# Optimization experiments

Hardware: AMD Instinct MI355X
Metric: run time of the kernel (lower is better)

## Reference

```python
import jax, jax.numpy as jnp
import numpy as np

QUERY_DIM = 512
KV_DIM = 64
N_AUX = 8
B = 65536
EPS = 1e-5


def setup_inputs() -> dict:
    key = jax.random.key(0)
    k1, k2, k3, k4, k5 = jax.random.split(key, 5)
    query = jax.random.normal(k1, (B, QUERY_DIM), dtype=jnp.float32)
    kv_stack = jax.random.normal(k2, (B, N_AUX, KV_DIM), dtype=jnp.float32)
    # Linear weights (torch nn.Linear stores W as [out, in]; y = x @ W.T)
    w_q = jax.random.normal(k3, (KV_DIM, QUERY_DIM), dtype=jnp.float32) / np.sqrt(QUERY_DIM)
    w_k = jax.random.normal(k4, (KV_DIM, KV_DIM), dtype=jnp.float32) / np.sqrt(KV_DIM)
    w_v = jax.random.normal(k5, (KV_DIM, KV_DIM), dtype=jnp.float32) / np.sqrt(KV_DIM)
    ln_gamma = jnp.ones((KV_DIM,), dtype=jnp.float32)
    ln_beta = jnp.zeros((KV_DIM,), dtype=jnp.float32)
    return {"query": query, "kv_stack": kv_stack, "w_q": w_q, "w_k": w_k,
            "w_v": w_v, "ln_gamma": ln_gamma, "ln_beta": ln_beta}


def reference(query, kv_stack, w_q, w_k, w_v, ln_gamma, ln_beta):
    scale = KV_DIM ** (-0.5)
    q = query @ w_q.T                                  # (B, kv_dim)
    k = jnp.einsum('bnd,ed->bne', kv_stack, w_k)       # (B, n_aux, kv_dim)
    v = jnp.einsum('bnd,ed->bne', kv_stack, w_v)       # (B, n_aux, kv_dim)
    scores = jnp.einsum('bd,bnd->bn', q, k) * scale    # (B, n_aux)
    attn_w = jax.nn.softmax(scores, axis=-1)
    out = jnp.einsum('bn,bnd->bd', attn_w, v)          # (B, kv_dim)
    # LayerNorm over last dim
    mu = jnp.mean(out, axis=-1, keepdims=True)
    var = jnp.var(out, axis=-1, keepdims=True)
    normed = (out - mu) / jnp.sqrt(var + EPS)
    return normed * ln_gamma + ln_beta
```

## Files before the change

### kernel.cpp

```cpp
#include <hip/hip_runtime.h>

#define QD 512
#define KD 64
#define NROWS 64
#define LDA 136
#define LDT 68
#define LDU 72

typedef __attribute__((ext_vector_type(8))) short short8;
typedef __attribute__((ext_vector_type(4))) float f32x4;
typedef __attribute__((ext_vector_type(4))) unsigned short u16x4;

static __device__ __forceinline__ unsigned short f2bf(float f) {
  unsigned u = __builtin_bit_cast(unsigned, f);
  u += 0x7FFFu + ((u >> 16) & 1u);
  return (unsigned short)(u >> 16);
}
static __device__ __forceinline__ float bf2f(unsigned short s) {
  return __builtin_bit_cast(float, (unsigned)s << 16);
}
static __device__ __forceinline__ short8 pack8(f32x4 a, f32x4 b) {
  short8 r;
  r[0] = (short)f2bf(a[0]); r[1] = (short)f2bf(a[1]);
  r[2] = (short)f2bf(a[2]); r[3] = (short)f2bf(a[3]);
  r[4] = (short)f2bf(b[0]); r[5] = (short)f2bf(b[1]);
  r[6] = (short)f2bf(b[2]); r[7] = (short)f2bf(b[3]);
  return r;
}

__global__ __launch_bounds__(256) void prep_kernel(
    const float* __restrict__ w_q, const float* __restrict__ w_k,
    const float* __restrict__ w_v, unsigned short* __restrict__ mt,
    unsigned short* __restrict__ wvb) {
  const int tid = (int)(blockIdx.x * 256 + threadIdx.x);
  if (tid < QD * KD) {
    const int c = tid >> 9;
    const int d = tid & 511;
    float acc = 0.f;
#pragma unroll 8
    for (int e = 0; e < 64; ++e)
      acc = fmaf(w_q[e * QD + d], w_k[e * KD + c], acc);
    mt[c * QD + d] = f2bf(acc);
  } else {
    const int i = tid - QD * KD;
    if (i < KD * KD) wvb[i] = f2bf(w_v[i]);
  }
}

__global__ __launch_bounds__(256, 3) void fused_kernel(
    const float* __restrict__ query,
    const float* __restrict__ kv,
    const unsigned short* __restrict__ mt,
    const unsigned short* __restrict__ wvb,
    const float* __restrict__ gamma,
    const float* __restrict__ beta,
    float* __restrict__ out) {
  __shared__ unsigned short lds_A[NROWS * LDA];
  __shared__ float lds_t[NROWS * LDT];
  __shared__ unsigned short lds_u[NROWS * LDU];

  const int tid  = (int)threadIdx.x;
  const int w    = tid >> 6;
  const int l    = tid & 63;
  const int m    = l & 15;
  const int quad = l >> 4;
  const long b0  = (long)blockIdx.x * NROWS;

  short8 bfrag[16];
  {
    const unsigned short* mp = mt + (w * 16 + m) * QD + quad * 8;
#pragma unroll
    for (int ks = 0; ks < 16; ++ks)
      bfrag[ks] = *(const short8*)(mp + ks * 32);
  }

  f32x4 acc[4];
#pragma unroll
  for (int rt = 0; rt < 4; ++rt) acc[rt] = (f32x4){0.f, 0.f, 0.f, 0.f};

  const int srow = tid >> 2;
  const int cseg = tid & 3;
  const float* qbase = query + (b0 + srow) * QD + cseg * 32;
  unsigned short* abase = lds_A + srow * LDA + cseg * 32;

  f32x4 stg[8];
#pragma unroll
  for (int i = 0; i < 8; ++i) stg[i] = *(const f32x4*)(qbase + i * 4);

#pragma unroll
  for (int kc = 0; kc < 4; ++kc) {
#pragma unroll
    for (int i = 0; i < 8; ++i)
      *(u16x4*)(abase + i * 4) = (u16x4){f2bf(stg[i][0]), f2bf(stg[i][1]),
                                         f2bf(stg[i][2]), f2bf(stg[i][3])};
    __syncthreads();
    if (kc < 3) {
      const float* nq = qbase + (kc + 1) * 128;
#pragma unroll
      for (int i = 0; i < 8; ++i) stg[i] = *(const f32x4*)(nq + i * 4);
    }
#pragma unroll
    for (int ks2 = 0; ks2 < 4; ++ks2) {
#pragma unroll
      for (int rt = 0; rt < 4; ++rt) {
        short8 af = *(const short8*)(lds_A + (rt * 16 + m) * LDA + ks2 * 32 + quad * 8);
        acc[rt] = __builtin_amdgcn_mfma_f32_16x16x32_bf16(af, bfrag[kc * 4 + ks2],
                                                          acc[rt], 0, 0, 0);
      }
    }
    __syncthreads();
  }

#pragma unroll
  for (int rt = 0; rt < 4; ++rt)
#pragma unroll
    for (int r2 = 0; r2 < 4; ++r2)
      lds_t[(rt * 16 + quad * 4 + r2) * LDT + w * 16 + m] = acc[rt][r2];
  __syncthreads();

  const int r  = w * 16 + m;
  const int q4 = quad;
  const long brow = b0 + r;

  const float* tp = lds_t + r * LDT + q4 * 16;
  f32x4 tv0 = ((const f32x4*)tp)[0];
  f32x4 tv1 = ((const f32x4*)tp)[1];
  f32x4 tv2 = ((const f32x4*)tp)[2];
  f32x4 tv3 = ((const f32x4*)tp)[3];

  float s[8];
  short8 kvb[8][2];
#pragma unroll
  for (int n = 0; n < 8; ++n) {
    const float* kp = kv + (brow * 8 + n) * 64 + q4 * 16;
    f32x4 k0 = ((const f32x4*)kp)[0];
    f32x4 k1 = ((const f32x4*)kp)[1];
    f32x4 k2 = ((const f32x4*)kp)[2];
    f32x4 k3 = ((const f32x4*)kp)[3];
    f32x4 d = tv0 * k0 + tv1 * k1 + tv2 * k2 + tv3 * k3;
    s[n] = d[0] + d[1] + d[2] + d[3];
    kvb[n][0] = pack8(k0, k1);
    kvb[n][1] = pack8(k2, k3);
  }
#pragma unroll
  for (int n = 0; n < 8; ++n) {
    s[n] += __shfl_xor(s[n], 16, 64);
    s[n] += __shfl_xor(s[n], 32, 64);
  }
  float mx = s[0];
#pragma unroll
  for (int n = 1; n < 8; ++n) mx = fmaxf(mx, s[n]);
  float ev[8];
  float esum = 0.f;
#pragma unroll
  for (int n = 0; n < 8; ++n) { ev[n] = __expf((s[n] - mx) * 0.125f); esum += ev[n]; }
  const float rinv = 1.0f / esum;

  f32x4 u0 = {0.f,0.f,0.f,0.f}, u1 = u0, u2 = u0, u3 = u0;
#pragma unroll
  for (int n = 0; n < 8; ++n) {
    const float a = ev[n];
    short8 p0 = kvb[n][0], p1 = kvb[n][1];
    u0 += a * (f32x4){bf2f((unsigned short)p0[0]), bf2f((unsigned short)p0[1]),
                      bf2f((unsigned short)p0[2]), bf2f((unsigned short)p0[3])};
    u1 += a * (f32x4){bf2f((unsigned short)p0[4]), bf2f((unsigned short)p0[5]),
                      bf2f((unsigned short)p0[6]), bf2f((unsigned short)p0[7])};
    u2 += a * (f32x4){bf2f((unsigned short)p1[0]), bf2f((unsigned short)p1[1]),
                      bf2f((unsigned short)p1[2]), bf2f((unsigned short)p1[3])};
    u3 += a * (f32x4){bf2f((unsigned short)p1[4]), bf2f((unsigned short)p1[5]),
                      bf2f((unsigned short)p1[6]), bf2f((unsigned short)p1[7])};
  }
  u0 *= rinv; u1 *= rinv; u2 *= rinv; u3 *= rinv;
  {
    unsigned short* up = lds_u + r * LDU + q4 * 16;
    *(short8*)(up)     = pack8(u0, u1);
    *(short8*)(up + 8) = pack8(u2, u3);
  }
  __syncthreads();

  short8 wvf0 = *(const short8*)(wvb + (w * 16 + m) * 64 + quad * 8);
  short8 wvf1 = *(const short8*)(wvb + (w * 16 + m) * 64 + 32 + quad * 8);
  f32x4 o[4];
#pragma unroll
  for (int rt = 0; rt < 4; ++rt) o[rt] = (f32x4){0.f, 0.f, 0.f, 0.f};
#pragma unroll
  for (int rt = 0; rt < 4; ++rt) {
    short8 a0 = *(const short8*)(lds_u + (rt * 16 + m) * LDU + quad * 8);
    o[rt] = __builtin_amdgcn_mfma_f32_16x16x32_bf16(a0, wvf0, o[rt], 0, 0, 0);
    short8 a1 = *(const short8*)(lds_u + (rt * 16 + m) * LDU + 32 + quad * 8);
    o[rt] = __builtin_amdgcn_mfma_f32_16x16x32_bf16(a1, wvf1, o[rt], 0, 0, 0);
  }
#pragma unroll
  for (int rt = 0; rt < 4; ++rt)
#pragma unroll
    for (int r2 = 0; r2 < 4; ++r2)
      lds_t[(rt * 16 + quad * 4 + r2) * LDT + w * 16 + m] = o[rt][r2];
  __syncthreads();

  const float* op = lds_t + r * LDT + q4 * 16;
  f32x4 x0 = ((const f32x4*)op)[0];
  f32x4 x1 = ((const f32x4*)op)[1];
  f32x4 x2 = ((const f32x4*)op)[2];
  f32x4 x3 = ((const f32x4*)op)[3];
  f32x4 sv = x0 + x1 + x2 + x3;
  f32x4 sq = x0 * x0 + x1 * x1 + x2 * x2 + x3 * x3;
  float s1 = sv[0] + sv[1] + sv[2] + sv[3];
  float s2 = sq[0] + sq[1] + sq[2] + sq[3];
  s1 += __shfl_xor(s1, 16, 64); s1 += __shfl_xor(s1, 32, 64);
  s2 += __shfl_xor(s2, 16, 64); s2 += __shfl_xor(s2, 32, 64);
  const float mu   = s1 * 0.015625f;
  const float var  = s2 * 0.015625f - mu * mu;
  const float rstd = rsqrtf(var + 1e-5f);
  const float* gp = gamma + q4 * 16;
  const float* bp = beta + q4 * 16;
  float* dst = out + brow * 64 + q4 * 16;
  {
    f32x4 g0 = ((const f32x4*)gp)[0], g1 = ((const f32x4*)gp)[1];
    f32x4 g2 = ((const f32x4*)gp)[2], g3 = ((const f32x4*)gp)[3];
    f32x4 e0 = ((const f32x4*)bp)[0], e1 = ((const f32x4*)bp)[1];
    f32x4 e2 = ((const f32x4*)bp)[2], e3 = ((const f32x4*)bp)[3];
    ((f32x4*)dst)[0] = (x0 - mu) * rstd * g0 + e0;
    ((f32x4*)dst)[1] = (x1 - mu) * rstd * g1 + e1;
    ((f32x4*)dst)[2] = (x2 - mu) * rstd * g2 + e2;
    ((f32x4*)dst)[3] = (x3 - mu) * rstd * g3 + e3;
  }
}

extern "C" void kernel_launch(void* const* d_in, const int* in_sizes, int n_in,
                              void* d_out, int out_size, void* d_ws, size_t ws_size,
                              hipStream_t stream) {
  const float* query = (const float*)d_in[0];
  const float* kv    = (const float*)d_in[1];
  const float* w_q   = (const float*)d_in[2];
  const float* w_k   = (const float*)d_in[3];
  const float* w_v   = (const float*)d_in[4];
  const float* gamma = (const float*)d_in[5];
  const float* beta  = (const float*)d_in[6];
  float* out = (float*)d_out;

  unsigned short* mt  = (unsigned short*)d_ws;
  unsigned short* wvb = mt + QD * KD;

  const int Bn = in_sizes[0] / QD;

  prep_kernel<<<(QD * KD + KD * KD + 255) / 256, 256, 0, stream>>>(w_q, w_k, w_v, mt, wvb);
  fused_kernel<<<Bn / NROWS, 256, 0, stream>>>(query, kv, mt, wvb, gamma, beta, out);
}
```

Measured before the change: 300.5 us.

## Halve rows per block, alias LDS buffers, and use 8 lanes per row

Each block now handles 32 rows instead of 64. The query staging and lds_t buffers share one LDS region, and the attention/LayerNorm phase maps 8 lanes to each row instead of 4, which shrinks per-thread register and LDS footprint. Launch bounds rise to 6 blocks per SU to raise occupancy and hide memory latency on this bandwidth-bound kernel. The cost is twice as many blocks, each reloading the 16 B-fragments of mt into registers, plus an extra shuffle step per reduction.

```diff
diff --git a/kernel.cpp b/kernel.cpp
--- a/kernel.cpp
+++ b/kernel.cpp
@@ -2,7 +2,7 @@
 
 #define QD 512
 #define KD 64
-#define NROWS 64
+#define NR 32
 #define LDA 136
 #define LDT 68
 #define LDU 72
@@ -47,7 +47,7 @@
   }
 }
 
-__global__ __launch_bounds__(256, 3) void fused_kernel(
+__global__ __launch_bounds__(256, 6) void fused_kernel(
     const float* __restrict__ query,
     const float* __restrict__ kv,
     const unsigned short* __restrict__ mt,
@@ -55,16 +55,17 @@
     const float* __restrict__ gamma,
     const float* __restrict__ beta,
     float* __restrict__ out) {
-  __shared__ unsigned short lds_A[NROWS * LDA];
-  __shared__ float lds_t[NROWS * LDT];
-  __shared__ unsigned short lds_u[NROWS * LDU];
+  __shared__ char shbuf[NR * LDA * 2];
+  unsigned short* lds_A = (unsigned short*)shbuf;
+  float* lds_t = (float*)shbuf;
+  __shared__ unsigned short lds_u[NR * LDU];
 
   const int tid  = (int)threadIdx.x;
   const int w    = tid >> 6;
   const int l    = tid & 63;
   const int m    = l & 15;
   const int quad = l >> 4;
-  const long b0  = (long)blockIdx.x * NROWS;
+  const long b0  = (long)blockIdx.x * NR;
 
   short8 bfrag[16];
   {
@@ -74,35 +75,35 @@
       bfrag[ks] = *(const short8*)(mp + ks * 32);
   }
 
-  f32x4 acc[4];
-#pragma unroll
-  for (int rt = 0; rt < 4; ++rt) acc[rt] = (f32x4){0.f, 0.f, 0.f, 0.f};
-
-  const int srow = tid >> 2;
-  const int cseg = tid & 3;
-  const float* qbase = query + (b0 + srow) * QD + cseg * 32;
-  unsigned short* abase = lds_A + srow * LDA + cseg * 32;
-
-  f32x4 stg[8];
-#pragma unroll
-  for (int i = 0; i < 8; ++i) stg[i] = *(const f32x4*)(qbase + i * 4);
+  f32x4 acc[2];
+  acc[0] = (f32x4){0.f, 0.f, 0.f, 0.f};
+  acc[1] = (f32x4){0.f, 0.f, 0.f, 0.f};
+
+  const int srow = tid >> 3;
+  const int cseg = tid & 7;
+  const float* qbase = query + (b0 + srow) * QD + cseg * 16;
+  unsigned short* abase = lds_A + srow * LDA + cseg * 16;
+
+  f32x4 stg[4];
+#pragma unroll
+  for (int i = 0; i < 4; ++i) stg[i] = *(const f32x4*)(qbase + i * 4);
 
 #pragma unroll
   for (int kc = 0; kc < 4; ++kc) {
 #pragma unroll
-    for (int i = 0; i < 8; ++i)
+    for (int i = 0; i < 4; ++i)
       *(u16x4*)(abase + i * 4) = (u16x4){f2bf(stg[i][0]), f2bf(stg[i][1]),
                                          f2bf(stg[i][2]), f2bf(stg[i][3])};
     __syncthreads();
     if (kc < 3) {
       const float* nq = qbase + (kc + 1) * 128;
 #pragma unroll
-      for (int i = 0; i < 8; ++i) stg[i] = *(const f32x4*)(nq + i * 4);
+      for (int i = 0; i < 4; ++i) stg[i] = *(const f32x4*)(nq + i * 4);
     }
 #pragma unroll
     for (int ks2 = 0; ks2 < 4; ++ks2) {
 #pragma unroll
-      for (int rt = 0; rt < 4; ++rt) {
+      for (int rt = 0; rt < 2; ++rt) {
         short8 af = *(const short8*)(lds_A + (rt * 16 + m) * LDA + ks2 * 32 + quad * 8);
         acc[rt] = __builtin_amdgcn_mfma_f32_16x16x32_bf16(af, bfrag[kc * 4 + ks2],
                                                           acc[rt], 0, 0, 0);
@@ -112,40 +113,37 @@
   }
 
 #pragma unroll
-  for (int rt = 0; rt < 4; ++rt)
+  for (int rt = 0; rt < 2; ++rt)
 #pragma unroll
     for (int r2 = 0; r2 < 4; ++r2)
       lds_t[(rt * 16 + quad * 4 + r2) * LDT + w * 16 + m] = acc[rt][r2];
   __syncthreads();
 
-  const int r  = w * 16 + m;
-  const int q4 = quad;
-  const long brow = b0 + r;
-
-  const float* tp = lds_t + r * LDT + q4 * 16;
+  const int rl = w * 8 + (l >> 3);
+  const int o8 = l & 7;
+  const int db = o8 * 8;
+  const long brow = b0 + rl;
+
+  const float* tp = lds_t + rl * LDT + db;
   f32x4 tv0 = ((const f32x4*)tp)[0];
   f32x4 tv1 = ((const f32x4*)tp)[1];
-  f32x4 tv2 = ((const f32x4*)tp)[2];
-  f32x4 tv3 = ((const f32x4*)tp)[3];
 
   float s[8];
-  short8 kvb[8][2];
+  short8 kvb[8];
 #pragma unroll
   for (int n = 0; n < 8; ++n) {
-    const float* kp = kv + (brow * 8 + n) * 64 + q4 * 16;
+    const float* kp = kv + (brow * 8 + n) * 64 + db;
     f32x4 k0 = ((const f32x4*)kp)[0];
     f32x4 k1 = ((const f32x4*)kp)[1];
-    f32x4 k2 = ((const f32x4*)kp)[2];
-    f32x4 k3 = ((const f32x4*)kp)[3];
-    f32x4 d = tv0 * k0 + tv1 * k1 + tv2 * k2 + tv3 * k3;
+    f32x4 d = tv0 * k0 + tv1 * k1;
     s[n] = d[0] + d[1] + d[2] + d[3];
-    kvb[n][0] = pack8(k0, k1);
-    kvb[n][1] = pack8(k2, k3);
+    kvb[n] = pack8(k0, k1);
   }
 #pragma unroll
   for (int n = 0; n < 8; ++n) {
-    s[n] += __shfl_xor(s[n], 16, 64);
-    s[n] += __shfl_xor(s[n], 32, 64);
+    s[n] += __shfl_xor(s[n], 1, 64);
+    s[n] += __shfl_xor(s[n], 2, 64);
+    s[n] += __shfl_xor(s[n], 4, 64);
   }
   float mx = s[0];
 #pragma unroll
@@ -156,73 +154,59 @@
   for (int n = 0; n < 8; ++n) { ev[n] = __expf((s[n] - mx) * 0.125f); esum += ev[n]; }
   const float rinv = 1.0f / esum;
 
-  f32x4 u0 = {0.f,0.f,0.f,0.f}, u1 = u0, u2 = u0, u3 = u0;
+  f32x4 u0 = {0.f, 0.f, 0.f, 0.f}, u1 = u0;
 #pragma unroll
   for (int n = 0; n < 8; ++n) {
     const float a = ev[n];
-    short8 p0 = kvb[n][0], p1 = kvb[n][1];
-    u0 += a * (f32x4){bf2f((unsigned short)p0[0]), bf2f((unsigned short)p0[1]),
-                      bf2f((unsigned short)p0[2]), bf2f((unsigned short)p0[3])};
-    u1 += a * (f32x4){bf2f((unsigned short)p0[4]), bf2f((unsigned short)p0[5]),
-                      bf2f((unsigned short)p0[6]), bf2f((unsigned short)p0[7])};
-    u2 += a * (f32x4){bf2f((unsigned short)p1[0]), bf2f((unsigned short)p1[1]),
-                      bf2f((unsigned short)p1[2]), bf2f((unsigned short)p1[3])};
-    u3 += a * (f32x4){bf2f((unsigned short)p1[4]), bf2f((unsigned short)p1[5]),
-                      bf2f((unsigned short)p1[6]), bf2f((unsigned short)p1[7])};
-  }
-  u0 *= rinv; u1 *= rinv; u2 *= rinv; u3 *= rinv;
-  {
-    unsigned short* up = lds_u + r * LDU + q4 * 16;
-    *(short8*)(up)     = pack8(u0, u1);
-    *(short8*)(up + 8) = pack8(u2, u3);
-  }
+    short8 p = kvb[n];
+    u0 += a * (f32x4){bf2f((unsigned short)p[0]), bf2f((unsigned short)p[1]),
+                      bf2f((unsigned short)p[2]), bf2f((unsigned short)p[3])};
+    u1 += a * (f32x4){bf2f((unsigned short)p[4]), bf2f((unsigned short)p[5]),
+                      bf2f((unsigned short)p[6]), bf2f((unsigned short)p[7])};
+  }
+  u0 *= rinv; u1 *= rinv;
+  *(short8*)(lds_u + rl * LDU + db) = pack8(u0, u1);
   __syncthreads();
 
   short8 wvf0 = *(const short8*)(wvb + (w * 16 + m) * 64 + quad * 8);
   short8 wvf1 = *(const short8*)(wvb + (w * 16 + m) * 64 + 32 + quad * 8);
-  f32x4 o[4];
-#pragma unroll
-  for (int rt = 0; rt < 4; ++rt) o[rt] = (f32x4){0.f, 0.f, 0.f, 0.f};
-#pragma unroll
-  for (int rt = 0; rt < 4; ++rt) {
+  f32x4 o[2];
+  o[0] = (f32x4){0.f, 0.f, 0.f, 0.f};
+  o[1] = (f32x4){0.f, 0.f, 0.f, 0.f};
+#pragma unroll
+  for (int rt = 0; rt < 2; ++rt) {
     short8 a0 = *(const short8*)(lds_u + (rt * 16 + m) * LDU + quad * 8);
     o[rt] = __builtin_amdgcn_mfma_f32_16x16x32_bf16(a0, wvf0, o[rt], 0, 0, 0);
     short8 a1 = *(const short8*)(lds_u + (rt * 16 + m) * LDU + 32 + quad * 8);
     o[rt] = __builtin_amdgcn_mfma_f32_16x16x32_bf16(a1, wvf1, o[rt], 0, 0, 0);
   }
 #pragma unroll
-  for (int rt = 0; rt < 4; ++rt)
+  for (int rt = 0; rt < 2; ++rt)
 #pragma unroll
     for (int r2 = 0; r2 < 4; ++r2)
       lds_t[(rt * 16 + quad * 4 + r2) * LDT + w * 16 + m] = o[rt][r2];
   __syncthreads();
 
-  const float* op = lds_t + r * LDT + q4 * 16;
+  const float* op = lds_t + rl * LDT + db;
   f32x4 x0 = ((const f32x4*)op)[0];
   f32x4 x1 = ((const f32x4*)op)[1];
-  f32x4 x2 = ((const f32x4*)op)[2];
-  f32x4 x3 = ((const f32x4*)op)[3];
-  f32x4 sv = x0 + x1 + x2 + x3;
-  f32x4 sq = x0 * x0 + x1 * x1 + x2 * x2 + x3 * x3;
+  f32x4 sv = x0 + x1;
+  f32x4 sq = x0 * x0 + x1 * x1;
   float s1 = sv[0] + sv[1] + sv[2] + sv[3];
   float s2 = sq[0] + sq[1] + sq[2] + sq[3];
-  s1 += __shfl_xor(s1, 16, 64); s1 += __shfl_xor(s1, 32, 64);
-  s2 += __shfl_xor(s2, 16, 64); s2 += __shfl_xor(s2, 32, 64);
+  s1 += __shfl_xor(s1, 1, 64); s1 += __shfl_xor(s1, 2, 64); s1 += __shfl_xor(s1, 4, 64);
+  s2 += __shfl_xor(s2, 1, 64); s2 += __shfl_xor(s2, 2, 64); s2 += __shfl_xor(s2, 4, 64);
   const float mu   = s1 * 0.015625f;
   const float var  = s2 * 0.015625f - mu * mu;
   const float rstd = rsqrtf(var + 1e-5f);
-  const float* gp = gamma + q4 * 16;
-  const float* bp = beta + q4 * 16;
-  float* dst = out + brow * 64 + q4 * 16;
+  const float* gp = gamma + db;
+  const float* bp = beta + db;
+  float* dst = out + brow * 64 + db;
   {
     f32x4 g0 = ((const f32x4*)gp)[0], g1 = ((const f32x4*)gp)[1];
-    f32x4 g2 = ((const f32x4*)gp)[2], g3 = ((const f32x4*)gp)[3];
     f32x4 e0 = ((const f32x4*)bp)[0], e1 = ((const f32x4*)bp)[1];
-    f32x4 e2 = ((const f32x4*)bp)[2], e3 = ((const f32x4*)bp)[3];
     ((f32x4*)dst)[0] = (x0 - mu) * rstd * g0 + e0;
     ((f32x4*)dst)[1] = (x1 - mu) * rstd * g1 + e1;
-    ((f32x4*)dst)[2] = (x2 - mu) * rstd * g2 + e2;
-    ((f32x4*)dst)[3] = (x3 - mu) * rstd * g3 + e3;
   }
 }
 
@@ -244,5 +228,5 @@
   const int Bn = in_sizes[0] / QD;
 
   prep_kernel<<<(QD * KD + KD * KD + 255) / 256, 256, 0, stream>>>(w_q, w_k, w_v, mt, wvb);
-  fused_kernel<<<Bn / NROWS, 256, 0, stream>>>(query, kv, mt, wvb, gamma, beta, out);
-}
+  fused_kernel<<<Bn / NR, 256, 0, stream>>>(query, kv, mt, wvb, gamma, beta, out);
+}
```

Result: slower. 316.3 us (+5.2%).
